# Performance work log

Measured on AMD Instinct MI355X. Metric: run time of the kernel, lower is better.

Reference implementation:

```python
import jax, jax.numpy as jnp
import numpy as np

B, L, T, H, NL, DFF, DIN = 4096, 64, 256, 8, 4, 1024, 6
HD = T // H
EPS = 1e-9


def setup_inputs() -> dict:
    key = jax.random.key(0)
    ks = jax.random.split(key, 12)
    s = 0.02
    inp = {
        "link_states": jax.random.uniform(ks[0], (B, L, DIN), jnp.float32) * 10.0,
        "link_W1": jax.random.normal(ks[1], (L, DIN, T), jnp.float32) * s,
        "link_b1": jnp.zeros((L, T), jnp.float32),
        "link_W2": jax.random.normal(ks[2], (L, T, T), jnp.float32) * s,
        "link_b2": jnp.zeros((L, T), jnp.float32),
        "Wqkv": jax.random.normal(ks[3], (NL, 3 * T, T), jnp.float32) * s,
        "bqkv": jnp.zeros((NL, 3 * T), jnp.float32),
        "Wo": jax.random.normal(ks[4], (NL, T, T), jnp.float32) * s,
        "bo": jnp.zeros((NL, T), jnp.float32),
        "ln1_g": jnp.ones((NL, T), jnp.float32),
        "ln1_b": jnp.zeros((NL, T), jnp.float32),
        "Wff1": jax.random.normal(ks[5], (NL, DFF, T), jnp.float32) * s,
        "bff1": jnp.zeros((NL, DFF), jnp.float32),
        "Wff2": jax.random.normal(ks[6], (NL, T, DFF), jnp.float32) * s,
        "bff2": jnp.zeros((NL, T), jnp.float32),
        "ln2_g": jnp.ones((NL, T), jnp.float32),
        "ln2_b": jnp.zeros((NL, T), jnp.float32),
        "head_W1": jax.random.normal(ks[7], (T, T), jnp.float32) * s,
        "head_b1": jnp.zeros((T,), jnp.float32),
        "head_W2": jax.random.normal(ks[8], (T, 1), jnp.float32) * s,
        "head_b2": jnp.zeros((1,), jnp.float32),
    }
    return inp


def _layernorm(x, g, b):
    m = x.mean(-1, keepdims=True)
    v = ((x - m) ** 2).mean(-1, keepdims=True)
    return (x - m) * jax.lax.rsqrt(v + 1e-5) * g + b


def _normalize_inputs(x):
    # x: [B, L, 6]
    prop = jnp.clip(x[:, :, 0], 0.0)
    tx = jnp.clip(x[:, :, 1], 0.0)
    sum_pt = prop + tx
    # torch.median returns lower-middle element for even L
    t_ref = jnp.sort(sum_pt, axis=1)[:, (L - 1) // 2][:, None]
    t_ref = jnp.clip(t_ref, 1e-6)
    f0 = prop / t_ref
    f1 = tx / t_ref
    f2 = x[:, :, 2]
    f3 = jnp.log1p(jnp.clip(x[:, :, 3], 0.0))
    f4 = jnp.log1p(jnp.clip(x[:, :, 4], 0.0) / t_ref)
    f5 = jnp.log1p(jnp.clip(x[:, :, 5], 0.0))
    head5 = jnp.stack([f0, f1, f2, f3, f4], axis=-1)  # [B,L,5]
    mean_a = head5.mean(axis=1, keepdims=True)
    std_a = head5.std(axis=1, keepdims=True) + EPS
    head5 = jnp.clip(head5, mean_a - 3.0 * std_a, mean_a + 3.0 * std_a)
    mean = head5.mean(axis=1, keepdims=True)
    std = head5.std(axis=1, keepdims=True) + EPS
    head5 = (head5 - mean) / std
    return jnp.concatenate([head5, f5[:, :, None]], axis=-1)


def _posenc():
    pos = jnp.arange(L, dtype=jnp.float32)[:, None]
    div = jnp.exp(-jnp.log(10000.0) * jnp.arange(0, T, 2, dtype=jnp.float32) / T)
    pe = jnp.zeros((L, T), jnp.float32)
    pe = pe.at[:, 0::2].set(jnp.sin(pos * div))
    pe = pe.at[:, 1::2].set(jnp.cos(pos * div))
    return pe


def _forward(link_states, link_W1, link_b1, link_W2, link_b2, Wqkv, bqkv, Wo, bo,
             ln1_g, ln1_b, Wff1, bff1, Wff2, bff2, ln2_g, ln2_b,
             head_W1, head_b1, head_W2, head_b2):
    x = _normalize_inputs(link_states)  # [B,L,6]
    # per-link (unshared) MLP encoders, batched as grouped matmuls
    h = jax.nn.relu(jnp.einsum('bld,ldt->blt', x, link_W1) + link_b1)
    tok = jnp.einsum('blt,lts->bls', h, link_W2) + link_b2  # [B,L,T]
    y = tok + _posenc()
    scale = 1.0 / np.sqrt(HD)
    for l in range(NL):
        qkv = y @ Wqkv[l].T + bqkv[l]  # [B,L,3T]
        q, k, v = jnp.split(qkv, 3, axis=-1)
        q = q.reshape(B, L, H, HD).transpose(0, 2, 1, 3)
        k = k.reshape(B, L, H, HD).transpose(0, 2, 1, 3)
        v = v.reshape(B, L, H, HD).transpose(0, 2, 1, 3)
        attn = jax.nn.softmax(jnp.einsum('bhqd,bhkd->bhqk', q, k) * scale, axis=-1)
        o = jnp.einsum('bhqk,bhkd->bhqd', attn, v).transpose(0, 2, 1, 3).reshape(B, L, T)
        o = o @ Wo[l].T + bo[l]
        y = _layernorm(y + o, ln1_g[l], ln1_b[l])
        ff = jax.nn.relu(y @ Wff1[l].T + bff1[l]) @ Wff2[l].T + bff2[l]
        y = _layernorm(y + ff, ln2_g[l], ln2_b[l])
    pooled = y.mean(axis=1)  # [B,T]
    hh = jax.nn.relu(pooled @ head_W1 + head_b1)
    values = (hh @ head_W2 + head_b2)[:, 0]  # [B]
    return values


def reference(link_states, link_W1, link_b1, link_W2, link_b2, Wqkv, bqkv, Wo, bo,
              ln1_g, ln1_b, Wff1, bff1, Wff2, bff2, ln2_g, ln2_b,
              head_W1, head_b1, head_W2, head_b2):
    return _forward(link_states, link_W1, link_b1, link_W2, link_b2, Wqkv, bqkv, Wo, bo,
                    ln1_g, ln1_b, Wff1, bff1, Wff2, bff2, ln2_g, ln2_b,
                    head_W1, head_b1, head_W2, head_b2)
```

## Files before the change

### kernel.cpp

```cpp
#include <hip/hip_runtime.h>
#include <cstddef>

#define B_   4096
#define L_   64
#define T_   256
#define H_   8
#define HD_  32
#define NL_  4
#define DFF_ 1024
#define DIN_ 6

typedef unsigned short ushort_t;
typedef __attribute__((ext_vector_type(8))) short bf16x8;
typedef __attribute__((ext_vector_type(4))) float f32x4;

__device__ __forceinline__ float wred_sum(float v) {
#pragma unroll
  for (int off = 32; off >= 1; off >>= 1) v += __shfl_xor(v, off, 64);
  return v;
}
__device__ __forceinline__ ushort_t f2bf(float f) {
  unsigned u = __builtin_bit_cast(unsigned, f);
  u += 0x7fffu + ((u >> 16) & 1u);
  return (ushort_t)(u >> 16);
}
__device__ __forceinline__ float bf2f(ushort_t h) {
  unsigned u = ((unsigned)h) << 16;
  return __builtin_bit_cast(float, u);
}
__device__ __forceinline__ void gl16(const ushort_t* g, const ushort_t* l) {
  __builtin_amdgcn_global_load_lds(
      (const __attribute__((address_space(1))) unsigned int*)g,
      (__attribute__((address_space(3))) unsigned int*)l, 16, 0, 0);
}

__global__ __launch_bounds__(64) void normalize_k(const float* __restrict__ xs,
                                                  float* __restrict__ xn) {
  const int b = blockIdx.x;
  const int l = threadIdx.x;
  const float* x = xs + ((size_t)b * L_ + l) * DIN_;
  const float x0 = x[0], x1 = x[1], x2 = x[2], x3 = x[3], x4 = x[4], x5 = x[5];
  const float prop = fmaxf(x0, 0.f), tx = fmaxf(x1, 0.f);
  const float sp = prop + tx;

  __shared__ float sh[64];
  __shared__ float med_sh;
  sh[l] = sp;
  __syncthreads();
  int rk = 0;
#pragma unroll 8
  for (int j = 0; j < 64; ++j) {
    const float vj = sh[j];
    rk += (vj < sp) || (vj == sp && j < l);
  }
  if (rk == 31) med_sh = sp;
  __syncthreads();
  const float t_ref = fmaxf(med_sh, 1e-6f);

  float f[5];
  f[0] = prop / t_ref;
  f[1] = tx / t_ref;
  f[2] = x2;
  f[3] = log1pf(fmaxf(x3, 0.f));
  f[4] = log1pf(fmaxf(x4, 0.f) / t_ref);
  const float f5 = log1pf(fmaxf(x5, 0.f));

  float* dst = xn + ((size_t)b * L_ + l) * DIN_;
#pragma unroll
  for (int i = 0; i < 5; ++i) {
    float v = f[i];
    float m = wred_sum(v) * (1.f / 64.f);
    float d = v - m;
    float sd = sqrtf(wred_sum(d * d) * (1.f / 64.f)) + 1e-9f;
    const float lo = m - 3.f * sd, hi = m + 3.f * sd;
    const float cv = fminf(fmaxf(v, lo), hi);
    const float m2 = wred_sum(cv) * (1.f / 64.f);
    const float d2 = cv - m2;
    const float sd2 = sqrtf(wred_sum(d2 * d2) * (1.f / 64.f)) + 1e-9f;
    dst[i] = (cv - m2) / sd2;
  }
  dst[5] = f5;
}

__global__ void pe_k(float* __restrict__ pe) {
  const int l = blockIdx.x;
  const int i = threadIdx.x;
  const float div = expf(-9.210340371976184f * (2.0f * i) / 256.0f);
  const float ang = (float)l * div;
  pe[l * T_ + 2 * i]     = sinf(ang);
  pe[l * T_ + 2 * i + 1] = cosf(ang);
}

__global__ void wfrag_k(const float* __restrict__ in, ushort_t* __restrict__ out,
                        int NK, int ksh) {
  const size_t z = blockIdx.z;
  const int idx = blockIdx.x * 256 + threadIdx.x;
  if (idx >= NK) return;
  const int e = idx & 7, li = (idx >> 3) & 15, t = idx >> 7;
  const int ks = t & ((1 << ksh) - 1), cb = t >> ksh;
  const int K = 8 << ksh;
  out[z * (size_t)NK + idx] =
      f2bf(in[z * (size_t)NK + (size_t)(cb * 16 + li) * K + ks * 8 + e]);
}

__global__ void w2t_k(const float* __restrict__ in, ushort_t* __restrict__ out) {
  const int idx = blockIdx.x * 256 + threadIdx.x;
  const int l = idx >> 16, r = idx & 65535, s = r >> 8, t = r & 255;
  out[idx] = f2bf(in[(l << 16) | (t << 8) | s]);
}

__global__ __launch_bounds__(256) void link1_k(const float* __restrict__ xn,
                                               const float* __restrict__ W1,
                                               const float* __restrict__ b1,
                                               ushort_t* __restrict__ h) {
  const size_t bl = blockIdx.x;
  const int l = (int)(bl & (L_ - 1));
  const int t = threadIdx.x;
  const float* x = xn + bl * DIN_;
  float a = b1[l * T_ + t];
#pragma unroll
  for (int d = 0; d < DIN_; ++d)
    a = fmaf(x[d], W1[((size_t)l * DIN_ + d) * T_ + t], a);
  h[bl * T_ + t] = f2bf(fmaxf(a, 0.f));
}

__global__ __launch_bounds__(512) void linkgemm_k(
    const ushort_t* __restrict__ A,
    const ushort_t* __restrict__ W,
    const float* __restrict__ bias,
    const float* __restrict__ pe,
    float* __restrict__ y32, ushort_t* __restrict__ y16o) {
  __shared__ ushort_t lA[2][4096];
  __shared__ ushort_t lB[2][8192];
  const int tid = threadIdx.x;
  const int lane = tid & 63, w = tid >> 6;
  const int wr = w >> 2, wc = w & 3;
  const size_t b0 = (size_t)blockIdx.x * 128;
  const int l = blockIdx.z;
  const ushort_t* Az = A + b0 * 16384 + (size_t)l * 256;
  const ushort_t* Wz = W + (size_t)l * 65536;

  const int sm = tid >> 6, sks = (tid >> 4) & 3, srr = tid & 15;

  auto stage = [&](int buf, int kt) {
    gl16(Az + (size_t)(16 * sm + srr) * 16384 + kt + sks * 8,
         &lA[buf][(tid & ~63) * 8]);
#pragma unroll
    for (int rd = 0; rd < 2; ++rd) {
      const int nb = sm + rd * 8;
      gl16(Wz + (size_t)(nb * 16 + srr) * 256 + kt + sks * 8,
           &lB[buf][rd * 4096 + (tid & ~63) * 8]);
    }
  };

  f32x4 acc[4][4];
#pragma unroll
  for (int mi = 0; mi < 4; ++mi)
#pragma unroll
    for (int ni = 0; ni < 4; ++ni) acc[mi][ni] = (f32x4){0.f, 0.f, 0.f, 0.f};

  stage(0, 0);
  asm volatile("s_waitcnt vmcnt(0)" ::: "memory");
  __syncthreads();
  int cur = 0;
  for (int t = 0; t < 8; ++t) {
    if (t + 1 < 8) stage(cur ^ 1, (t + 1) << 5);
    bf16x8 af[4], bfr[4];
#pragma unroll
    for (int mi = 0; mi < 4; ++mi)
      af[mi] = *(const bf16x8*)&lA[cur][((wr * 4 + mi) * 64 + lane) * 8];
#pragma unroll
    for (int ni = 0; ni < 4; ++ni)
      bfr[ni] = *(const bf16x8*)&lB[cur][((wc * 4 + ni) * 64 + lane) * 8];
#pragma unroll
    for (int mi = 0; mi < 4; ++mi)
#pragma unroll
      for (int ni = 0; ni < 4; ++ni)
        acc[mi][ni] = __builtin_amdgcn_mfma_f32_16x16x32_bf16(
            af[mi], bfr[ni], acc[mi][ni], 0, 0, 0);
    asm volatile("s_waitcnt vmcnt(0)" ::: "memory");
    __syncthreads();
    cur ^= 1;
  }

  const int r_in = (lane >> 4) * 4;
  const int c_in = lane & 15;
#pragma unroll
  for (int ni = 0; ni < 4; ++ni) {
    const int cg = wc * 64 + ni * 16 + c_in;
    const float bs = bias[l * 256 + cg] + pe[l * 256 + cg];
#pragma unroll
    for (int mi = 0; mi < 4; ++mi) {
#pragma unroll
      for (int rg = 0; rg < 4; ++rg) {
        const size_t bg = b0 + wr * 64 + mi * 16 + r_in + rg;
        const float v = acc[mi][ni][rg] + bs;
        y32[bg * 16384 + l * 256 + cg] = v;
        y16o[bg * 16384 + l * 256 + cg] = f2bf(v);
      }
    }
  }
}

__global__ __launch_bounds__(256, 2) void attnblk_k(
    const ushort_t* __restrict__ yin,
    const ushort_t* __restrict__ Wq, const float* __restrict__ bqkv,
    const ushort_t* __restrict__ Wo, const float* __restrict__ bo,
    const float* __restrict__ lng, const float* __restrict__ lnb,
    float* __restrict__ y32, ushort_t* __restrict__ y16o) {
  __shared__ ushort_t yF[16384];
  __shared__ ushort_t buf1[4][2304];
  __shared__ ushort_t vT[4][2304];
  __shared__ float red[4][2][64];
  const int b = blockIdx.x;
  const int tid = threadIdx.x, lane = tid & 63, w = tid >> 6;
  const int li = lane & 15, g = lane >> 4;
  const size_t row0 = (size_t)b * 64;
  const float scale = 0.17677669529663687f;

#pragma unroll
  for (int j = 0; j < 8; ++j) {
    const int u = j * 256 + tid;
    const int row = u & 63, ks = u >> 6;
    const uint4 v = *(const uint4*)(yin + (row0 + row) * 256 + ks * 8);
    *(uint4*)&yF[(((row >> 4) * 32 + ks) * 16 + (row & 15)) * 8] = v;
  }
  __syncthreads();

  f32x4 oa2[2][4][2];
#pragma unroll
  for (int hi = 0; hi < 2; ++hi) {
    const int h = w * 2 + hi, hoff = h * 32;

    f32x4 acc[3][2][4];
#pragma unroll
    for (int m = 0; m < 3; ++m)
#pragma unroll
      for (int n = 0; n < 2; ++n)
#pragma unroll
        for (int mi = 0; mi < 4; ++mi) acc[m][n][mi] = (f32x4){0.f, 0.f, 0.f, 0.f};
#pragma unroll
    for (int kt = 0; kt < 8; ++kt) {
      bf16x8 af[4];
#pragma unroll
      for (int mi = 0; mi < 4; ++mi)
        af[mi] = *(const bf16x8*)&yF[((mi * 32 + kt * 4 + g) * 16 + li) * 8];
      bf16x8 bw[3][2];
#pragma unroll
      for (int m = 0; m < 3; ++m)
#pragma unroll
        for (int n = 0; n < 2; ++n)
          bw[m][n] = *(const bf16x8*)(Wq +
              (size_t)(((m * 16 + 2 * h + n) * 32 + kt * 4 + g) * 16 + li) * 8);
#pragma unroll
      for (int m = 0; m < 3; ++m)
#pragma unroll
        for (int n = 0; n < 2; ++n)
#pragma unroll
          for (int mi = 0; mi < 4; ++mi)
            acc[m][n][mi] = __builtin_amdgcn_mfma_f32_16x16x32_bf16(
                af[mi], bw[m][n], acc[m][n][mi], 0, 0, 0);
    }
    float bs[3][2];
#pragma unroll
    for (int m = 0; m < 3; ++m)
#pragma unroll
      for (int n = 0; n < 2; ++n) bs[m][n] = bqkv[m * 256 + hoff + 16 * n + li];

#pragma unroll
    for (int n = 0; n < 2; ++n)
#pragma unroll
      for (int mi = 0; mi < 4; ++mi)
#pragma unroll
        for (int r = 0; r < 4; ++r)
          buf1[w][(16 * mi + 4 * g + r) * 36 + 16 * n + li] =
              f2bf(acc[0][n][mi][r] + bs[0][n]);
    bf16x8 qb[4];
#pragma unroll
    for (int ni = 0; ni < 4; ++ni)
      qb[ni] = *(const bf16x8*)&buf1[w][(16 * ni + li) * 36 + g * 8];

#pragma unroll
    for (int n = 0; n < 2; ++n)
#pragma unroll
      for (int mi = 0; mi < 4; ++mi)
#pragma unroll
        for (int r = 0; r < 4; ++r)
          buf1[w][(16 * mi + 4 * g + r) * 36 + 16 * n + li] =
              f2bf(acc[1][n][mi][r] + bs[1][n]);
    bf16x8 ka[4];
#pragma unroll
    for (int mi = 0; mi < 4; ++mi)
      ka[mi] = *(const bf16x8*)&buf1[w][(16 * mi + li) * 36 + g * 8];

#pragma unroll
    for (int n = 0; n < 2; ++n)
#pragma unroll
      for (int mi = 0; mi < 4; ++mi)
#pragma unroll
        for (int r = 0; r < 4; ++r)
          vT[w][(16 * n + li) * 72 + 16 * mi + 4 * g + r] =
              f2bf(acc[2][n][mi][r] + bs[2][n]);
    bf16x8 vb[2][2];
#pragma unroll
    for (int ks = 0; ks < 2; ++ks)
#pragma unroll
      for (int n2 = 0; n2 < 2; ++n2)
        vb[ks][n2] = *(const bf16x8*)&vT[w][(16 * n2 + li) * 72 + ks * 32 + g * 8];

#pragma unroll
    for (int mi = 0; mi < 4; ++mi)
#pragma unroll
      for (int n2 = 0; n2 < 2; ++n2) oa2[hi][mi][n2] = (f32x4){0.f, 0.f, 0.f, 0.f};

#pragma unroll
    for (int half = 0; half < 2; ++half) {
      f32x4 s[4][2];
#pragma unroll
      for (int mi = 0; mi < 4; ++mi)
#pragma unroll
        for (int nn = 0; nn < 2; ++nn)
          s[mi][nn] = __builtin_amdgcn_mfma_f32_16x16x32_bf16(
              ka[mi], qb[2 * half + nn], (f32x4){0.f, 0.f, 0.f, 0.f}, 0, 0, 0);

#pragma unroll
      for (int nn = 0; nn < 2; ++nn) {
        float mx = -3.4e38f;
#pragma unroll
        for (int mi = 0; mi < 4; ++mi)
#pragma unroll
          for (int r = 0; r < 4; ++r) {
            s[mi][nn][r] *= scale;
            mx = fmaxf(mx, s[mi][nn][r]);
          }
        mx = fmaxf(mx, __shfl_xor(mx, 16, 64));
        mx = fmaxf(mx, __shfl_xor(mx, 32, 64));
        float sum = 0.f;
#pragma unroll
        for (int mi = 0; mi < 4; ++mi)
#pragma unroll
          for (int r = 0; r < 4; ++r) {
            const float e = expf(s[mi][nn][r] - mx);
            s[mi][nn][r] = e;
            sum += e;
          }
        sum += __shfl_xor(sum, 16, 64);
        sum += __shfl_xor(sum, 32, 64);
        const float inv = 1.f / sum;
        const int qrow = 16 * nn + li;
#pragma unroll
        for (int mi = 0; mi < 4; ++mi) {
          unsigned lo = (unsigned)f2bf(s[mi][nn][0] * inv) |
                        ((unsigned)f2bf(s[mi][nn][1] * inv) << 16);
          unsigned hi2 = (unsigned)f2bf(s[mi][nn][2] * inv) |
                         ((unsigned)f2bf(s[mi][nn][3] * inv) << 16);
          *(uint2*)&buf1[w][qrow * 72 + 16 * mi + 4 * g] = make_uint2(lo, hi2);
        }
      }

#pragma unroll
      for (int ks = 0; ks < 2; ++ks) {
        bf16x8 pa[2];
#pragma unroll
        for (int m2 = 0; m2 < 2; ++m2)
          pa[m2] = *(const bf16x8*)&buf1[w][(16 * m2 + li) * 72 + ks * 32 + g * 8];
#pragma unroll
        for (int m2 = 0; m2 < 2; ++m2)
#pragma unroll
          for (int n2 = 0; n2 < 2; ++n2)
            oa2[hi][2 * half + m2][n2] = __builtin_amdgcn_mfma_f32_16x16x32_bf16(
                pa[m2], vb[ks][n2], oa2[hi][2 * half + m2][n2], 0, 0, 0);
      }
    }
  }

  __syncthreads();
#pragma unroll
  for (int hi = 0; hi < 2; ++hi) {
    const int hoff = (2 * w + hi) * 32;
#pragma unroll
    for (int mi = 0; mi < 4; ++mi)
#pragma unroll
      for (int n2 = 0; n2 < 2; ++n2)
#pragma unroll
        for (int r = 0; r < 4; ++r) {
          const int row = 16 * mi + 4 * g + r;
          const int col = hoff + 16 * n2 + li;
          yF[(((row >> 4) * 32 + (col >> 3)) * 16 + (row & 15)) * 8 + (col & 7)] =
              f2bf(oa2[hi][mi][n2][r]);
        }
  }
  __syncthreads();

  f32x4 acc[4][4];
#pragma unroll
  for (int mi = 0; mi < 4; ++mi)
#pragma unroll
    for (int ni = 0; ni < 4; ++ni) acc[mi][ni] = (f32x4){0.f, 0.f, 0.f, 0.f};
#pragma unroll
  for (int kt = 0; kt < 8; ++kt) {
    bf16x8 af[4], bfr[4];
#pragma unroll
    for (int mi = 0; mi < 4; ++mi)
      af[mi] = *(const bf16x8*)&yF[((mi * 32 + kt * 4 + g) * 16 + li) * 8];
#pragma unroll
    for (int ni = 0; ni < 4; ++ni)
      bfr[ni] = *(const bf16x8*)(Wo +
          (size_t)(((4 * w + ni) * 32 + kt * 4 + g) * 16 + li) * 8);
#pragma unroll
    for (int mi = 0; mi < 4; ++mi)
#pragma unroll
      for (int ni = 0; ni < 4; ++ni)
        acc[mi][ni] = __builtin_amdgcn_mfma_f32_16x16x32_bf16(
            af[mi], bfr[ni], acc[mi][ni], 0, 0, 0);
  }

  const int r_in = (lane >> 4) * 4;
  const int c_in = lane & 15;
#pragma unroll
  for (int mi = 0; mi < 4; ++mi) {
#pragma unroll
    for (int rg = 0; rg < 4; ++rg) {
      const int row_l = 16 * mi + r_in + rg;
      float s1 = 0.f, s2 = 0.f;
#pragma unroll
      for (int ni = 0; ni < 4; ++ni) {
        const int cg = 64 * w + 16 * ni + c_in;
        const float zv = acc[mi][ni][rg] + bo[cg] + y32[(row0 + row_l) * 256 + cg];
        acc[mi][ni][rg] = zv;
        s1 += zv;
        s2 += zv * zv;
      }
#pragma unroll
      for (int off = 1; off <= 8; off <<= 1) {
        s1 += __shfl_xor(s1, off, 64);
        s2 += __shfl_xor(s2, off, 64);
      }
      if (c_in == 0) {
        red[w][0][row_l] = s1;
        red[w][1][row_l] = s2;
      }
    }
  }
  __syncthreads();
#pragma unroll
  for (int mi = 0; mi < 4; ++mi) {
#pragma unroll
    for (int rg = 0; rg < 4; ++rg) {
      const int row_l = 16 * mi + r_in + rg;
      const float S1 = red[0][0][row_l] + red[1][0][row_l] + red[2][0][row_l] + red[3][0][row_l];
      const float S2 = red[0][1][row_l] + red[1][1][row_l] + red[2][1][row_l] + red[3][1][row_l];
      const float m = S1 * (1.f / 256.f);
      const float var = S2 * (1.f / 256.f) - m * m;
      const float rs = rsqrtf(var + 1e-5f);
#pragma unroll
      for (int ni = 0; ni < 4; ++ni) {
        const int cg = 64 * w + 16 * ni + c_in;
        const float v = (acc[mi][ni][rg] - m) * rs * lng[cg] + lnb[cg];
        y32[(row0 + row_l) * 256 + cg] = v;
        y16o[(row0 + row_l) * 256 + cg] = f2bf(v);
      }
    }
  }
}

__global__ __launch_bounds__(512, 4) void ffblk_k(
    const ushort_t* __restrict__ yin,
    const ushort_t* __restrict__ W1,
    const ushort_t* __restrict__ W2,
    const float* __restrict__ b1, const float* __restrict__ b2,
    const float* __restrict__ lng, const float* __restrict__ lnb,
    float* __restrict__ y32, ushort_t* __restrict__ y16o) {
  __shared__ ushort_t yF[16384];
  __shared__ ushort_t zF[16384];
  __shared__ float red[8][2][64];
  const int tid = threadIdx.x;
  const int lane = tid & 63, w = tid >> 6;
  const int li = lane & 15, g = lane >> 4;
  const size_t row0 = (size_t)blockIdx.x * 64;

#pragma unroll
  for (int j = 0; j < 4; ++j) {
    const int u = j * 512 + tid;
    const int row = u & 63, ks = u >> 6;
    const uint4 v = *(const uint4*)(yin + (row0 + row) * 256 + ks * 8);
    *(uint4*)&yF[(((row >> 4) * 32 + ks) * 16 + (row & 15)) * 8] = v;
  }
  __syncthreads();

  f32x4 acc2[4][2];
#pragma unroll
  for (int mi = 0; mi < 4; ++mi)
#pragma unroll
    for (int n = 0; n < 2; ++n) acc2[mi][n] = (f32x4){0.f, 0.f, 0.f, 0.f};

#pragma unroll 1
  for (int q = 0; q < 4; ++q) {
    f32x4 acc1[4][2];
#pragma unroll
    for (int mi = 0; mi < 4; ++mi)
#pragma unroll
      for (int n = 0; n < 2; ++n) acc1[mi][n] = (f32x4){0.f, 0.f, 0.f, 0.f};
#pragma unroll
    for (int kt = 0; kt < 8; ++kt) {
      bf16x8 af[4], bw[2];
#pragma unroll
      for (int mi = 0; mi < 4; ++mi)
        af[mi] = *(const bf16x8*)&yF[((mi * 32 + kt * 4 + g) * 16 + li) * 8];
#pragma unroll
      for (int n = 0; n < 2; ++n)
        bw[n] = *(const bf16x8*)(W1 +
            (size_t)(((16 * q + 2 * w + n) * 32 + kt * 4 + g) * 16 + li) * 8);
#pragma unroll
      for (int mi = 0; mi < 4; ++mi)
#pragma unroll
        for (int n = 0; n < 2; ++n)
          acc1[mi][n] = __builtin_amdgcn_mfma_f32_16x16x32_bf16(
              af[mi], bw[n], acc1[mi][n], 0, 0, 0);
    }
    if (q) __syncthreads();
#pragma unroll
    for (int n = 0; n < 2; ++n) {
      const int kk = 32 * w + 16 * n + li;
      const float bb = b1[256 * q + kk];
#pragma unroll
      for (int mi = 0; mi < 4; ++mi)
#pragma unroll
        for (int r = 0; r < 4; ++r) {
          const int row = 16 * mi + 4 * g + r;
          zF[(((row >> 4) * 32 + (kk >> 3)) * 16 + (row & 15)) * 8 + (kk & 7)] =
              f2bf(fmaxf(acc1[mi][n][r] + bb, 0.f));
        }
    }
    __syncthreads();
#pragma unroll
    for (int kt = 0; kt < 8; ++kt) {
      bf16x8 af2[4], bw2[2];
#pragma unroll
      for (int mi = 0; mi < 4; ++mi)
        af2[mi] = *(const bf16x8*)&zF[((mi * 32 + kt * 4 + g) * 16 + li) * 8];
#pragma unroll
      for (int n = 0; n < 2; ++n)
        bw2[n] = *(const bf16x8*)(W2 +
            (size_t)(((2 * w + n) * 128 + 32 * q + kt * 4 + g) * 16 + li) * 8);
#pragma unroll
      for (int mi = 0; mi < 4; ++mi)
#pragma unroll
        for (int n = 0; n < 2; ++n)
          acc2[mi][n] = __builtin_amdgcn_mfma_f32_16x16x32_bf16(
              af2[mi], bw2[n], acc2[mi][n], 0, 0, 0);
    }
  }

  const int r_in = (lane >> 4) * 4;
  const int c_in = lane & 15;
#pragma unroll
  for (int mi = 0; mi < 4; ++mi) {
#pragma unroll
    for (int rg = 0; rg < 4; ++rg) {
      const int row_l = 16 * mi + r_in + rg;
      float s1 = 0.f, s2 = 0.f;
#pragma unroll
      for (int n = 0; n < 2; ++n) {
        const int cg = 32 * w + 16 * n + c_in;
        const float zv = acc2[mi][n][rg] + b2[cg] + y32[(row0 + row_l) * 256 + cg];
        acc2[mi][n][rg] = zv;
        s1 += zv;
        s2 += zv * zv;
      }
#pragma unroll
      for (int off = 1; off <= 8; off <<= 1) {
        s1 += __shfl_xor(s1, off, 64);
        s2 += __shfl_xor(s2, off, 64);
      }
      if (c_in == 0) {
        red[w][0][row_l] = s1;
        red[w][1][row_l] = s2;
      }
    }
  }
  __syncthreads();
#pragma unroll
  for (int mi = 0; mi < 4; ++mi) {
#pragma unroll
    for (int rg = 0; rg < 4; ++rg) {
      const int row_l = 16 * mi + r_in + rg;
      float S1 = 0.f, S2 = 0.f;
#pragma unroll
      for (int ww = 0; ww < 8; ++ww) {
        S1 += red[ww][0][row_l];
        S2 += red[ww][1][row_l];
      }
      const float m = S1 * (1.f / 256.f);
      const float var = S2 * (1.f / 256.f) - m * m;
      const float rs = rsqrtf(var + 1e-5f);
#pragma unroll
      for (int n = 0; n < 2; ++n) {
        const int cg = 32 * w + 16 * n + c_in;
        const float v = (acc2[mi][n][rg] - m) * rs * lng[cg] + lnb[cg];
        y32[(row0 + row_l) * 256 + cg] = v;
        y16o[(row0 + row_l) * 256 + cg] = f2bf(v);
      }
    }
  }
}

__global__ __launch_bounds__(256) void pooled_k(const float* __restrict__ y,
                                                float* __restrict__ pooled) {
  const size_t b = blockIdx.x;
  const int t = threadIdx.x;
  const float* p = y + b * (L_ * T_) + t;
  float s = 0.f;
#pragma unroll
  for (int l = 0; l < L_; ++l) s += p[l * T_];
  pooled[b * T_ + t] = s * (1.f / 64.f);
}

__global__ __launch_bounds__(256) void headgemm_k(
    const float* __restrict__ A, const float* __restrict__ Wt,
    const float* __restrict__ bias, float* __restrict__ out) {
  const int tid = threadIdx.x;
  const int tx = tid & 63, ty = tid >> 6;
  const int cfull = tx * 4;
  const size_t b0 = (size_t)blockIdx.x * 64;

  __shared__ float At[256][68];

  float4 acc[16];
#pragma unroll
  for (int r = 0; r < 16; ++r) acc[r] = make_float4(0.f, 0.f, 0.f, 0.f);
  const int r0 = ty * 16;

  {
    const int rr = tid >> 6;
    const int k4 = (tid & 63) * 4;
#pragma unroll
    for (int p = 0; p < 16; ++p) {
      const int r = p * 4 + rr;
      const float4 v = *(const float4*)(A + (b0 + r) * 256 + k4);
      At[k4 + 0][r] = v.x;
      At[k4 + 1][r] = v.y;
      At[k4 + 2][r] = v.z;
      At[k4 + 3][r] = v.w;
    }
  }
  __syncthreads();
  const float* wp = Wt + cfull;
#pragma unroll 2
  for (int k = 0; k < 256; ++k) {
    const float4 w = *(const float4*)wp;
    wp += 256;
    const float4* ar = (const float4*)(&At[k][r0]);
    const float4 a0 = ar[0], a1 = ar[1], a2 = ar[2], a3 = ar[3];
    const float av[16] = {a0.x, a0.y, a0.z, a0.w, a1.x, a1.y, a1.z, a1.w,
                          a2.x, a2.y, a2.z, a2.w, a3.x, a3.y, a3.z, a3.w};
#pragma unroll
    for (int r = 0; r < 16; ++r) {
      acc[r].x = fmaf(av[r], w.x, acc[r].x);
      acc[r].y = fmaf(av[r], w.y, acc[r].y);
      acc[r].z = fmaf(av[r], w.z, acc[r].z);
      acc[r].w = fmaf(av[r], w.w, acc[r].w);
    }
  }
  const float4 bb = *(const float4*)(bias + cfull);
#pragma unroll
  for (int r = 0; r < 16; ++r) {
    const size_t row = b0 + r0 + r;
    float4 o;
    o.x = fmaxf(acc[r].x + bb.x, 0.f);
    o.y = fmaxf(acc[r].y + bb.y, 0.f);
    o.z = fmaxf(acc[r].z + bb.z, 0.f);
    o.w = fmaxf(acc[r].w + bb.w, 0.f);
    *(float4*)(out + row * 256 + cfull) = o;
  }
}

__global__ __launch_bounds__(64) void head2_k(const float* __restrict__ hh,
                                              const float* __restrict__ W2,
                                              const float* __restrict__ b2,
                                              float* __restrict__ out) {
  const size_t b = blockIdx.x;
  const int lane = threadIdx.x;
  const float4 hv = *(const float4*)(hh + b * T_ + lane * 4);
  const float4 wv = *(const float4*)(W2 + lane * 4);
  float s = hv.x * wv.x + hv.y * wv.y + hv.z * wv.z + hv.w * wv.w;
  s = wred_sum(s);
  if (lane == 0) out[b] = s + b2[0];
}

extern "C" void kernel_launch(void* const* d_in, const int* in_sizes, int n_in,
                              void* d_out, int out_size, void* d_ws, size_t ws_size,
                              hipStream_t stream) {
  const float* link_states = (const float*)d_in[0];
  const float* link_W1 = (const float*)d_in[1];
  const float* link_b1 = (const float*)d_in[2];
  const float* link_W2 = (const float*)d_in[3];
  const float* link_b2 = (const float*)d_in[4];
  const float* Wqkv = (const float*)d_in[5];
  const float* bqkv = (const float*)d_in[6];
  const float* Wo = (const float*)d_in[7];
  const float* bo = (const float*)d_in[8];
  const float* ln1_g = (const float*)d_in[9];
  const float* ln1_b = (const float*)d_in[10];
  const float* Wff1 = (const float*)d_in[11];
  const float* bff1 = (const float*)d_in[12];
  const float* Wff2 = (const float*)d_in[13];
  const float* bff2 = (const float*)d_in[14];
  const float* ln2_g = (const float*)d_in[15];
  const float* ln2_b = (const float*)d_in[16];
  const float* head_W1 = (const float*)d_in[17];
  const float* head_b1 = (const float*)d_in[18];
  const float* head_W2 = (const float*)d_in[19];
  const float* head_b2 = (const float*)d_in[20];

  char* base = (char*)d_ws;
  size_t off = 0;
  auto alloc = [&](size_t bytes) -> char* {
    char* p = base + off;
    off = (off + bytes + 255) & ~(size_t)255;
    return p;
  };

  ushort_t* Wqkv16 = (ushort_t*)alloc((size_t)NL_ * 768 * 256 * 2);
  ushort_t* Wo16   = (ushort_t*)alloc((size_t)NL_ * 256 * 256 * 2);
  ushort_t* Wff116 = (ushort_t*)alloc((size_t)NL_ * 1024 * 256 * 2);
  ushort_t* Wff216 = (ushort_t*)alloc((size_t)NL_ * 256 * 1024 * 2);
  ushort_t* W2T16  = (ushort_t*)alloc((size_t)L_ * 256 * 256 * 2);
  float* pe     = (float*)alloc((size_t)L_ * T_ * 4);
  float* xn     = (float*)alloc((size_t)B_ * L_ * DIN_ * 4);
  float* pooled = (float*)alloc((size_t)B_ * T_ * 4);
  float* hh     = (float*)alloc((size_t)B_ * T_ * 4);

  const size_t fixed_end = off;
  const size_t availB = (ws_size > fixed_end + 65536) ? (ws_size - fixed_end - 65536) : 0;
  int NC = 1;
  while (NC < 32 && (size_t)(B_ / NC) * 98304ull > availB) NC <<= 1;
  const int Bc = B_ / NC;

  float*    y32 = (float*)alloc((size_t)Bc * L_ * T_ * 4);
  ushort_t* y16 = (ushort_t*)alloc((size_t)Bc * L_ * T_ * 2);

  wfrag_k<<<dim3((768 * 256 + 255) / 256, 1, NL_), 256, 0, stream>>>(
      Wqkv, Wqkv16, 768 * 256, 5);
  wfrag_k<<<dim3((256 * 256 + 255) / 256, 1, NL_), 256, 0, stream>>>(
      Wo, Wo16, 256 * 256, 5);
  wfrag_k<<<dim3((1024 * 256 + 255) / 256, 1, NL_), 256, 0, stream>>>(
      Wff1, Wff116, 1024 * 256, 5);
  wfrag_k<<<dim3((256 * 1024 + 255) / 256, 1, NL_), 256, 0, stream>>>(
      Wff2, Wff216, 256 * 1024, 7);
  w2t_k<<<(L_ * 256 * 256) / 256, 256, 0, stream>>>(link_W2, W2T16);
  pe_k<<<L_, 128, 0, stream>>>(pe);
  normalize_k<<<B_, 64, 0, stream>>>(link_states, xn);

  for (int c = 0; c < NC; ++c) {
    const size_t bs = (size_t)c * Bc;

    link1_k<<<Bc * L_, 256, 0, stream>>>(xn + bs * L_ * DIN_, link_W1, link_b1, y16);
    linkgemm_k<<<dim3(Bc / 128, 1, L_), 512, 0, stream>>>(
        y16, W2T16, link_b2, pe, y32, y16);

    for (int l = 0; l < NL_; ++l) {
      attnblk_k<<<dim3(Bc, 1, 1), 256, 0, stream>>>(
          y16, Wqkv16 + (size_t)l * 768 * 256, bqkv + l * 768,
          Wo16 + (size_t)l * 256 * 256, bo + l * 256,
          ln1_g + l * 256, ln1_b + l * 256, y32, y16);
      ffblk_k<<<dim3(Bc, 1, 1), 512, 0, stream>>>(
          y16, Wff116 + (size_t)l * 1024 * 256, Wff216 + (size_t)l * 256 * 1024,
          bff1 + l * 1024, bff2 + l * 256,
          ln2_g + l * 256, ln2_b + l * 256, y32, y16);
    }

    pooled_k<<<Bc, 256, 0, stream>>>(y32, pooled + bs * T_);
  }

  headgemm_k<<<B_ / 64, 256, 0, stream>>>(pooled, head_W1, head_b1, hh);
  head2_k<<<B_, 64, 0, stream>>>(hh, head_W2, head_b2, (float*)d_out);
}
```

Before: 4.389 ms.

## Fuse attention and feed-forward blocks into one per-layer kernel

Merges the attention kernel and the feed-forward kernel into a single layer kernel per batch element. The post-attention LayerNorm output stays in registers and LDS, which removes a global round trip of the fp32 and bf16 activations between the two blocks. The separate bf16 activation copy is dropped: the kernel reads fp32 and converts to bf16 on load. In exchange the feed-forward part now runs with 256 threads (4 waves) instead of 512, so each wave does twice the work, and the scratch LDS is shared between the attention buffers and the FFN intermediate, which raises register pressure and may lower occupancy.

```diff
diff --git a/kernel.cpp b/kernel.cpp
--- a/kernel.cpp
+++ b/kernel.cpp
@@ -129,7 +129,7 @@
     const ushort_t* __restrict__ W,
     const float* __restrict__ bias,
     const float* __restrict__ pe,
-    float* __restrict__ y32, ushort_t* __restrict__ y16o) {
+    float* __restrict__ y32) {
   __shared__ ushort_t lA[2][4096];
   __shared__ ushort_t lB[2][8192];
   const int tid = threadIdx.x;
@@ -194,35 +194,46 @@
 #pragma unroll
       for (int rg = 0; rg < 4; ++rg) {
         const size_t bg = b0 + wr * 64 + mi * 16 + r_in + rg;
-        const float v = acc[mi][ni][rg] + bs;
-        y32[bg * 16384 + l * 256 + cg] = v;
-        y16o[bg * 16384 + l * 256 + cg] = f2bf(v);
-      }
-    }
-  }
-}
-
-__global__ __launch_bounds__(256, 2) void attnblk_k(
-    const ushort_t* __restrict__ yin,
+        y32[bg * 16384 + l * 256 + cg] = acc[mi][ni][rg] + bs;
+      }
+    }
+  }
+}
+
+__global__ __launch_bounds__(256, 2) void layer_k(
+    float* __restrict__ y32,
     const ushort_t* __restrict__ Wq, const float* __restrict__ bqkv,
     const ushort_t* __restrict__ Wo, const float* __restrict__ bo,
-    const float* __restrict__ lng, const float* __restrict__ lnb,
-    float* __restrict__ y32, ushort_t* __restrict__ y16o) {
+    const float* __restrict__ ln1g, const float* __restrict__ ln1b,
+    const ushort_t* __restrict__ Wf1, const float* __restrict__ bf1,
+    const ushort_t* __restrict__ Wf2, const float* __restrict__ bf2,
+    const float* __restrict__ ln2g, const float* __restrict__ ln2b) {
   __shared__ ushort_t yF[16384];
-  __shared__ ushort_t buf1[4][2304];
-  __shared__ ushort_t vT[4][2304];
+  __shared__ ushort_t sc[18432];
   __shared__ float red[4][2][64];
   const int b = blockIdx.x;
   const int tid = threadIdx.x, lane = tid & 63, w = tid >> 6;
   const int li = lane & 15, g = lane >> 4;
   const size_t row0 = (size_t)b * 64;
   const float scale = 0.17677669529663687f;
+  ushort_t* bufw = sc + w * 2304;
+  ushort_t* vtw  = sc + 9216 + w * 2304;
+  ushort_t* zF   = sc;
 
 #pragma unroll
   for (int j = 0; j < 8; ++j) {
     const int u = j * 256 + tid;
     const int row = u & 63, ks = u >> 6;
-    const uint4 v = *(const uint4*)(yin + (row0 + row) * 256 + ks * 8);
+    const float* src = y32 + (row0 + row) * 256 + ks * 8;
+    const float4 a = *(const float4*)src;
+    const float4 c = *(const float4*)(src + 4);
+    uint2 pk;
+    pk.x = (unsigned)f2bf(a.x) | ((unsigned)f2bf(a.y) << 16);
+    pk.y = (unsigned)f2bf(a.z) | ((unsigned)f2bf(a.w) << 16);
+    uint2 pk2;
+    pk2.x = (unsigned)f2bf(c.x) | ((unsigned)f2bf(c.y) << 16);
+    pk2.y = (unsigned)f2bf(c.z) | ((unsigned)f2bf(c.w) << 16);
+    uint4 v = make_uint4(pk.x, pk.y, pk2.x, pk2.y);
     *(uint4*)&yF[(((row >> 4) * 32 + ks) * 16 + (row & 15)) * 8] = v;
   }
   __syncthreads();
@@ -273,12 +284,12 @@
       for (int mi = 0; mi < 4; ++mi)
 #pragma unroll
         for (int r = 0; r < 4; ++r)
-          buf1[w][(16 * mi + 4 * g + r) * 36 + 16 * n + li] =
+          bufw[(16 * mi + 4 * g + r) * 36 + 16 * n + li] =
               f2bf(acc[0][n][mi][r] + bs[0][n]);
     bf16x8 qb[4];
 #pragma unroll
     for (int ni = 0; ni < 4; ++ni)
-      qb[ni] = *(const bf16x8*)&buf1[w][(16 * ni + li) * 36 + g * 8];
+      qb[ni] = *(const bf16x8*)&bufw[(16 * ni + li) * 36 + g * 8];
 
 #pragma unroll
     for (int n = 0; n < 2; ++n)
@@ -286,12 +297,12 @@
       for (int mi = 0; mi < 4; ++mi)
 #pragma unroll
         for (int r = 0; r < 4; ++r)
-          buf1[w][(16 * mi + 4 * g + r) * 36 + 16 * n + li] =
+          bufw[(16 * mi + 4 * g + r) * 36 + 16 * n + li] =
               f2bf(acc[1][n][mi][r] + bs[1][n]);
     bf16x8 ka[4];
 #pragma unroll
     for (int mi = 0; mi < 4; ++mi)
-      ka[mi] = *(const bf16x8*)&buf1[w][(16 * mi + li) * 36 + g * 8];
+      ka[mi] = *(const bf16x8*)&bufw[(16 * mi + li) * 36 + g * 8];
 
 #pragma unroll
     for (int n = 0; n < 2; ++n)
@@ -299,14 +310,14 @@
       for (int mi = 0; mi < 4; ++mi)
 #pragma unroll
         for (int r = 0; r < 4; ++r)
-          vT[w][(16 * n + li) * 72 + 16 * mi + 4 * g + r] =
+          vtw[(16 * n + li) * 72 + 16 * mi + 4 * g + r] =
               f2bf(acc[2][n][mi][r] + bs[2][n]);
     bf16x8 vb[2][2];
 #pragma unroll
     for (int ks = 0; ks < 2; ++ks)
 #pragma unroll
       for (int n2 = 0; n2 < 2; ++n2)
-        vb[ks][n2] = *(const bf16x8*)&vT[w][(16 * n2 + li) * 72 + ks * 32 + g * 8];
+        vb[ks][n2] = *(const bf16x8*)&vtw[(16 * n2 + li) * 72 + ks * 32 + g * 8];
 
 #pragma unroll
     for (int mi = 0; mi < 4; ++mi)
@@ -354,7 +365,7 @@
                         ((unsigned)f2bf(s[mi][nn][1] * inv) << 16);
           unsigned hi2 = (unsigned)f2bf(s[mi][nn][2] * inv) |
                          ((unsigned)f2bf(s[mi][nn][3] * inv) << 16);
-          *(uint2*)&buf1[w][qrow * 72 + 16 * mi + 4 * g] = make_uint2(lo, hi2);
+          *(uint2*)&bufw[qrow * 72 + 16 * mi + 4 * g] = make_uint2(lo, hi2);
         }
       }
 
@@ -363,7 +374,7 @@
         bf16x8 pa[2];
 #pragma unroll
         for (int m2 = 0; m2 < 2; ++m2)
-          pa[m2] = *(const bf16x8*)&buf1[w][(16 * m2 + li) * 72 + ks * 32 + g * 8];
+          pa[m2] = *(const bf16x8*)&bufw[(16 * m2 + li) * 72 + ks * 32 + g * 8];
 #pragma unroll
         for (int m2 = 0; m2 < 2; ++m2)
 #pragma unroll
@@ -417,6 +428,7 @@
 
   const int r_in = (lane >> 4) * 4;
   const int c_in = lane & 15;
+  float y1r[4][4][4];
 #pragma unroll
   for (int mi = 0; mi < 4; ++mi) {
 #pragma unroll
@@ -456,104 +468,82 @@
 #pragma unroll
       for (int ni = 0; ni < 4; ++ni) {
         const int cg = 64 * w + 16 * ni + c_in;
-        const float v = (acc[mi][ni][rg] - m) * rs * lng[cg] + lnb[cg];
-        y32[(row0 + row_l) * 256 + cg] = v;
-        y16o[(row0 + row_l) * 256 + cg] = f2bf(v);
-      }
-    }
-  }
-}
-
-__global__ __launch_bounds__(512, 4) void ffblk_k(
-    const ushort_t* __restrict__ yin,
-    const ushort_t* __restrict__ W1,
-    const ushort_t* __restrict__ W2,
-    const float* __restrict__ b1, const float* __restrict__ b2,
-    const float* __restrict__ lng, const float* __restrict__ lnb,
-    float* __restrict__ y32, ushort_t* __restrict__ y16o) {
-  __shared__ ushort_t yF[16384];
-  __shared__ ushort_t zF[16384];
-  __shared__ float red[8][2][64];
-  const int tid = threadIdx.x;
-  const int lane = tid & 63, w = tid >> 6;
-  const int li = lane & 15, g = lane >> 4;
-  const size_t row0 = (size_t)blockIdx.x * 64;
-
-#pragma unroll
-  for (int j = 0; j < 4; ++j) {
-    const int u = j * 512 + tid;
-    const int row = u & 63, ks = u >> 6;
-    const uint4 v = *(const uint4*)(yin + (row0 + row) * 256 + ks * 8);
-    *(uint4*)&yF[(((row >> 4) * 32 + ks) * 16 + (row & 15)) * 8] = v;
-  }
-  __syncthreads();
-
-  f32x4 acc2[4][2];
+        const float v = (acc[mi][ni][rg] - m) * rs * ln1g[cg] + ln1b[cg];
+        y1r[mi][ni][rg] = v;
+        yF[(((row_l >> 4) * 32 + (cg >> 3)) * 16 + (row_l & 15)) * 8 + (cg & 7)] =
+            f2bf(v);
+      }
+    }
+  }
+  __syncthreads();
+
+  f32x4 acc2[4][4];
 #pragma unroll
   for (int mi = 0; mi < 4; ++mi)
 #pragma unroll
-    for (int n = 0; n < 2; ++n) acc2[mi][n] = (f32x4){0.f, 0.f, 0.f, 0.f};
+    for (int ni = 0; ni < 4; ++ni) acc2[mi][ni] = (f32x4){0.f, 0.f, 0.f, 0.f};
 
 #pragma unroll 1
   for (int q = 0; q < 4; ++q) {
-    f32x4 acc1[4][2];
-#pragma unroll
-    for (int mi = 0; mi < 4; ++mi)
-#pragma unroll
-      for (int n = 0; n < 2; ++n) acc1[mi][n] = (f32x4){0.f, 0.f, 0.f, 0.f};
+#pragma unroll 1
+    for (int p = 0; p < 2; ++p) {
+      f32x4 acc1[4][2];
+#pragma unroll
+      for (int mi = 0; mi < 4; ++mi)
+#pragma unroll
+        for (int n = 0; n < 2; ++n) acc1[mi][n] = (f32x4){0.f, 0.f, 0.f, 0.f};
+#pragma unroll
+      for (int kt = 0; kt < 8; ++kt) {
+        bf16x8 af[4], bw[2];
+#pragma unroll
+        for (int mi = 0; mi < 4; ++mi)
+          af[mi] = *(const bf16x8*)&yF[((mi * 32 + kt * 4 + g) * 16 + li) * 8];
+#pragma unroll
+        for (int n = 0; n < 2; ++n)
+          bw[n] = *(const bf16x8*)(Wf1 +
+              (size_t)(((16 * q + 4 * w + 2 * p + n) * 32 + kt * 4 + g) * 16 + li) * 8);
+#pragma unroll
+        for (int mi = 0; mi < 4; ++mi)
+#pragma unroll
+          for (int n = 0; n < 2; ++n)
+            acc1[mi][n] = __builtin_amdgcn_mfma_f32_16x16x32_bf16(
+                af[mi], bw[n], acc1[mi][n], 0, 0, 0);
+      }
+      if (q && p == 0) __syncthreads();
+#pragma unroll
+      for (int n = 0; n < 2; ++n) {
+        const int kk = 64 * w + 32 * p + 16 * n + li;
+        const float bb = bf1[256 * q + kk];
+#pragma unroll
+        for (int mi = 0; mi < 4; ++mi)
+#pragma unroll
+          for (int r = 0; r < 4; ++r) {
+            const int row = 16 * mi + 4 * g + r;
+            zF[(((row >> 4) * 32 + (kk >> 3)) * 16 + (row & 15)) * 8 + (kk & 7)] =
+                f2bf(fmaxf(acc1[mi][n][r] + bb, 0.f));
+          }
+      }
+    }
+    __syncthreads();
 #pragma unroll
     for (int kt = 0; kt < 8; ++kt) {
-      bf16x8 af[4], bw[2];
-#pragma unroll
-      for (int mi = 0; mi < 4; ++mi)
-        af[mi] = *(const bf16x8*)&yF[((mi * 32 + kt * 4 + g) * 16 + li) * 8];
-#pragma unroll
-      for (int n = 0; n < 2; ++n)
-        bw[n] = *(const bf16x8*)(W1 +
-            (size_t)(((16 * q + 2 * w + n) * 32 + kt * 4 + g) * 16 + li) * 8);
-#pragma unroll
-      for (int mi = 0; mi < 4; ++mi)
-#pragma unroll
-        for (int n = 0; n < 2; ++n)
-          acc1[mi][n] = __builtin_amdgcn_mfma_f32_16x16x32_bf16(
-              af[mi], bw[n], acc1[mi][n], 0, 0, 0);
-    }
-    if (q) __syncthreads();
-#pragma unroll
-    for (int n = 0; n < 2; ++n) {
-      const int kk = 32 * w + 16 * n + li;
-      const float bb = b1[256 * q + kk];
-#pragma unroll
-      for (int mi = 0; mi < 4; ++mi)
-#pragma unroll
-        for (int r = 0; r < 4; ++r) {
-          const int row = 16 * mi + 4 * g + r;
-          zF[(((row >> 4) * 32 + (kk >> 3)) * 16 + (row & 15)) * 8 + (kk & 7)] =
-              f2bf(fmaxf(acc1[mi][n][r] + bb, 0.f));
-        }
-    }
-    __syncthreads();
-#pragma unroll
-    for (int kt = 0; kt < 8; ++kt) {
-      bf16x8 af2[4], bw2[2];
+      bf16x8 af2[4], bw2[4];
 #pragma unroll
       for (int mi = 0; mi < 4; ++mi)
         af2[mi] = *(const bf16x8*)&zF[((mi * 32 + kt * 4 + g) * 16 + li) * 8];
 #pragma unroll
-      for (int n = 0; n < 2; ++n)
-        bw2[n] = *(const bf16x8*)(W2 +
-            (size_t)(((2 * w + n) * 128 + 32 * q + kt * 4 + g) * 16 + li) * 8);
+      for (int ni = 0; ni < 4; ++ni)
+        bw2[ni] = *(const bf16x8*)(Wf2 +
+            (size_t)(((4 * w + ni) * 128 + 32 * q + kt * 4 + g) * 16 + li) * 8);
 #pragma unroll
       for (int mi = 0; mi < 4; ++mi)
 #pragma unroll
-        for (int n = 0; n < 2; ++n)
-          acc2[mi][n] = __builtin_amdgcn_mfma_f32_16x16x32_bf16(
-              af2[mi], bw2[n], acc2[mi][n], 0, 0, 0);
-    }
-  }
-
-  const int r_in = (lane >> 4) * 4;
-  const int c_in = lane & 15;
+        for (int ni = 0; ni < 4; ++ni)
+          acc2[mi][ni] = __builtin_amdgcn_mfma_f32_16x16x32_bf16(
+              af2[mi], bw2[ni], acc2[mi][ni], 0, 0, 0);
+    }
+  }
+
 #pragma unroll
   for (int mi = 0; mi < 4; ++mi) {
 #pragma unroll
@@ -561,10 +551,10 @@
       const int row_l = 16 * mi + r_in + rg;
       float s1 = 0.f, s2 = 0.f;
 #pragma unroll
-      for (int n = 0; n < 2; ++n) {
-        const int cg = 32 * w + 16 * n + c_in;
-        const float zv = acc2[mi][n][rg] + b2[cg] + y32[(row0 + row_l) * 256 + cg];
-        acc2[mi][n][rg] = zv;
+      for (int ni = 0; ni < 4; ++ni) {
+        const int cg = 64 * w + 16 * ni + c_in;
+        const float zv = acc2[mi][ni][rg] + bf2[cg] + y1r[mi][ni][rg];
+        acc2[mi][ni][rg] = zv;
         s1 += zv;
         s2 += zv * zv;
       }
@@ -585,21 +575,16 @@
 #pragma unroll
     for (int rg = 0; rg < 4; ++rg) {
       const int row_l = 16 * mi + r_in + rg;
-      float S1 = 0.f, S2 = 0.f;
-#pragma unroll
-      for (int ww = 0; ww < 8; ++ww) {
-        S1 += red[ww][0][row_l];
-        S2 += red[ww][1][row_l];
-      }
+      const float S1 = red[0][0][row_l] + red[1][0][row_l] + red[2][0][row_l] + red[3][0][row_l];
+      const float S2 = red[0][1][row_l] + red[1][1][row_l] + red[2][1][row_l] + red[3][1][row_l];
       const float m = S1 * (1.f / 256.f);
       const float var = S2 * (1.f / 256.f) - m * m;
       const float rs = rsqrtf(var + 1e-5f);
 #pragma unroll
-      for (int n = 0; n < 2; ++n) {
-        const int cg = 32 * w + 16 * n + c_in;
-        const float v = (acc2[mi][n][rg] - m) * rs * lng[cg] + lnb[cg];
-        y32[(row0 + row_l) * 256 + cg] = v;
-        y16o[(row0 + row_l) * 256 + cg] = f2bf(v);
+      for (int ni = 0; ni < 4; ++ni) {
+        const int cg = 64 * w + 16 * ni + c_in;
+        y32[(row0 + row_l) * 256 + cg] =
+            (acc2[mi][ni][rg] - m) * rs * ln2g[cg] + ln2b[cg];
       }
     }
   }
@@ -737,8 +722,8 @@
   while (NC < 32 && (size_t)(B_ / NC) * 98304ull > availB) NC <<= 1;
   const int Bc = B_ / NC;
 
-  float*    y32 = (float*)alloc((size_t)Bc * L_ * T_ * 4);
-  ushort_t* y16 = (ushort_t*)alloc((size_t)Bc * L_ * T_ * 2);
+  float*    y32  = (float*)alloc((size_t)Bc * L_ * T_ * 4);
+  ushort_t* hbuf = (ushort_t*)alloc((size_t)Bc * L_ * T_ * 2);
 
   wfrag_k<<<dim3((768 * 256 + 255) / 256, 1, NL_), 256, 0, stream>>>(
       Wqkv, Wqkv16, 768 * 256, 5);
@@ -755,19 +740,19 @@
   for (int c = 0; c < NC; ++c) {
     const size_t bs = (size_t)c * Bc;
 
-    link1_k<<<Bc * L_, 256, 0, stream>>>(xn + bs * L_ * DIN_, link_W1, link_b1, y16);
+    link1_k<<<Bc * L_, 256, 0, stream>>>(xn + bs * L_ * DIN_, link_W1, link_b1, hbuf);
     linkgemm_k<<<dim3(Bc / 128, 1, L_), 512, 0, stream>>>(
-        y16, W2T16, link_b2, pe, y32, y16);
+        hbuf, W2T16, link_b2, pe, y32);
 
     for (int l = 0; l < NL_; ++l) {
-      attnblk_k<<<dim3(Bc, 1, 1), 256, 0, stream>>>(
-          y16, Wqkv16 + (size_t)l * 768 * 256, bqkv + l * 768,
+      layer_k<<<dim3(Bc, 1, 1), 256, 0, stream>>>(
+          y32,
+          Wqkv16 + (size_t)l * 768 * 256, bqkv + l * 768,
           Wo16 + (size_t)l * 256 * 256, bo + l * 256,
-          ln1_g + l * 256, ln1_b + l * 256, y32, y16);
-      ffblk_k<<<dim3(Bc, 1, 1), 512, 0, stream>>>(
-          y16, Wff116 + (size_t)l * 1024 * 256, Wff216 + (size_t)l * 256 * 1024,
-          bff1 + l * 1024, bff2 + l * 256,
-          ln2_g + l * 256, ln2_b + l * 256, y32, y16);
+          ln1_g + l * 256, ln1_b + l * 256,
+          Wff116 + (size_t)l * 1024 * 256, bff1 + l * 1024,
+          Wff216 + (size_t)l * 256 * 1024, bff2 + l * 256,
+          ln2_g + l * 256, ln2_b + l * 256);
     }
 
     pooled_k<<<Bc, 256, 0, stream>>>(y32, pooled + bs * T_);
```

Result: faster. 3.712 ms (median of 2 runs) (-15.4%).
